# Optimization experiments

Hardware: AMD Instinct MI355X
Metric: run time of the kernel (lower is better)

Reference implementation:

```python
import jax, jax.numpy as jnp
import numpy as np

N_NODES = 50000
N_EDGES = 1600000
IN_DIM = 128
HID = 128
SHARED = 64
N_GRAPHS = 2048


def setup_inputs() -> dict:
    key = jax.random.key(0)
    ks = jax.random.split(key, 16)
    x = jax.random.normal(ks[0], (N_NODES, IN_DIM), dtype=jnp.float32)
    edge_index = jax.random.randint(ks[1], (2, N_EDGES), 0, N_NODES, dtype=jnp.int64)
    batch = jnp.sort(jax.random.randint(ks[2], (N_NODES,), 0, N_GRAPHS, dtype=jnp.int64))

    def lin(k, fan_in, fan_out):
        bound = 1.0 / np.sqrt(fan_in)
        kw, kb = jax.random.split(k)
        W = jax.random.uniform(kw, (fan_in, fan_out), minval=-bound, maxval=bound, dtype=jnp.float32)
        b = jax.random.uniform(kb, (fan_out,), minval=-bound, maxval=bound, dtype=jnp.float32)
        return W, b

    W1a, b1a = lin(ks[3], IN_DIM, HID)
    W1b, b1b = lin(ks[4], HID, HID)
    W2a, b2a = lin(ks[5], HID, HID)
    W2b, b2b = lin(ks[6], HID, HID)
    Ws, bs = lin(ks[7], HID, SHARED)
    WlS, blS = lin(ks[8], SHARED, 1)
    WlP, blP = lin(ks[9], SHARED, 1)
    WnR, bnR = lin(ks[10], SHARED, 1)
    return dict(x=x, edge_index=edge_index, batch=batch,
                W1a=W1a, b1a=b1a, W1b=W1b, b1b=b1b,
                W2a=W2a, b2a=b2a, W2b=W2b, b2b=b2b,
                Ws=Ws, bs=bs, WlS=WlS, blS=blS, WlP=WlP, blP=blP, WnR=WnR, bnR=bnR)


def gin_conv(x, src, dst, Wa, ba, Wb, bb):
    # GINConv (eps=0): h_i = MLP(x_i + sum_{j->i} x_j)
    agg = jax.ops.segment_sum(x[src], dst, num_segments=N_NODES)
    h = x + agg
    h = jax.nn.relu(h @ Wa + ba)
    return h @ Wb + bb


def reference(x, edge_index, batch, W1a, b1a, W1b, b1b, W2a, b2a, W2b, b2b,
              Ws, bs, WlS, blS, WlP, blP, WnR, bnR):
    src, dst = edge_index[0], edge_index[1]
    h = jax.nn.relu(gin_conv(x, src, dst, W1a, b1a, W1b, b1b))
    h = jax.nn.relu(gin_conv(h, src, dst, W2a, b2a, W2b, b2b))
    # global mean pool over graph ids
    sums = jax.ops.segment_sum(h, batch, num_segments=N_GRAPHS)
    counts = jax.ops.segment_sum(jnp.ones((h.shape[0],), h.dtype), batch, num_segments=N_GRAPHS)
    pooled = sums / jnp.maximum(counts, 1.0)[:, None]
    g = jax.nn.relu(pooled @ Ws + bs)
    out_logS = (g @ WlS + blS)[:, 0]
    out_logP = (g @ WlP + blP)[:, 0]
    out_NR = (g @ WnR + bnR)[:, 0]
    return (out_logS, out_logP, out_NR)
```

## Files before the change

kernel.cpp:

```cpp
#include <hip/hip_runtime.h>
#include <hip/hip_bf16.h>


#define IN_DIM 128
#define NFINE 128
#define BIN_EPB 4096
#define SRCCH 16
#define NSLOT 6400
#define SPT 13

typedef float  f32x4  __attribute__((ext_vector_type(4)));
typedef short  bf16x4 __attribute__((ext_vector_type(4)));
typedef short  bf16x8 __attribute__((ext_vector_type(8)));

__device__ __forceinline__ unsigned short bf16_rne(float v) {
    unsigned u = __float_as_uint(v);
    unsigned t = u + 0x7fffu + ((u >> 16) & 1u);
    return (unsigned short)(t >> 16);
}


__global__ __launch_bounds__(256) void f32_to_bf16_kernel(
    const float4* __restrict__ in, uint4* __restrict__ out, int n8)
{
    int i = blockIdx.x * 256 + threadIdx.x;
    if (i >= n8) return;
    float4 a = in[i * 2];
    float4 b = in[i * 2 + 1];
    float v[8] = {a.x, a.y, a.z, a.w, b.x, b.y, b.z, b.w};
    unsigned r[4];
#pragma unroll
    for (int j = 0; j < 4; ++j)
        r[j] = (unsigned)bf16_rne(v[j * 2]) | ((unsigned)bf16_rne(v[j * 2 + 1]) << 16);
    out[i] = make_uint4(r[0], r[1], r[2], r[3]);
}


__global__ __launch_bounds__(256) void conv_weights_kernel(
    const float* __restrict__ W0, const float* __restrict__ W1,
    const float* __restrict__ W2, const float* __restrict__ W3,
    unsigned short* __restrict__ Wh, unsigned short* __restrict__ Wl)
{
    int m   = blockIdx.x >> 6;
    int idx = (blockIdx.x & 63) * 256 + threadIdx.x;
    const float* W = (m == 0) ? W0 : (m == 1) ? W1 : (m == 2) ? W2 : W3;
    int k = idx >> 7, n = idx & 127;
    float v = W[idx];
    unsigned short hh = bf16_rne(v);
    float hf = __uint_as_float(((unsigned)hh) << 16);
    unsigned short ll = bf16_rne(v - hf);
    Wh[m * 16384 + n * 128 + k] = hh;
    Wl[m * 16384 + n * 128 + k] = ll;
}


__global__ __launch_bounds__(256) void bin_kernel(
    const int* __restrict__ src, const int* __restrict__ dst,
    int2* __restrict__ buckets, int* __restrict__ bcur,
    int n_edges, int n_nodes, int cap)
{
    __shared__ int cnt[NFINE];
    __shared__ int base[NFINE];
    for (int i = threadIdx.x; i < NFINE; i += 256) cnt[i] = 0;
    __syncthreads();

    const int e0 = blockIdx.x * BIN_EPB + threadIdx.x * 16;
    int ne = n_edges - e0;
    if (ne < 0) ne = 0;
    if (ne > 16) ne = 16;

    int d[16], s[16], off[16];
    if (ne == 16) {
#pragma unroll
        for (int q = 0; q < 4; ++q) {
            int4 dv = *(const int4*)(dst + e0 + q * 4);
            int4 sv = *(const int4*)(src + e0 + q * 4);
            d[q * 4 + 0] = dv.x; d[q * 4 + 1] = dv.y;
            d[q * 4 + 2] = dv.z; d[q * 4 + 3] = dv.w;
            s[q * 4 + 0] = sv.x; s[q * 4 + 1] = sv.y;
            s[q * 4 + 2] = sv.z; s[q * 4 + 3] = sv.w;
        }
    } else {
#pragma unroll
        for (int j = 0; j < 16; ++j) {
            d[j] = (j < ne) ? dst[e0 + j] : 0;
            s[j] = (j < ne) ? src[e0 + j] : 0;
        }
    }
#pragma unroll
    for (int j = 0; j < 16; ++j)
        if (j < ne) {
            int b = (int)(((long long)d[j] * NFINE) / n_nodes);
            off[j] = atomicAdd(&cnt[b], 1);
        }
    __syncthreads();
    for (int i = threadIdx.x; i < NFINE; i += 256)
        base[i] = atomicAdd(&bcur[i], cnt[i]);
    __syncthreads();
#pragma unroll
    for (int j = 0; j < 16; ++j)
        if (j < ne) {
            int b = (int)(((long long)d[j] * NFINE) / n_nodes);
            buckets[(size_t)b * cap + base[b] + off[j]] = make_int2(d[j], s[j]);
        }
}

__global__ __launch_bounds__(512) void csr_fused_kernel(
    const int2* __restrict__ buckets, const int* __restrict__ bcnt,
    int* __restrict__ row_start, int* __restrict__ csr_src,
    int cap, int n_nodes, int n_edges)
{
    __shared__ int bc[NFINE];
    __shared__ int h[NSLOT];
    __shared__ int tsum[512];
    __shared__ int bbase_s;

    const int b = blockIdx.x;
    const int t = threadIdx.x;
    const int lo_n = (int)(((long long)b * n_nodes + NFINE - 1) / NFINE);
    const int hi_n = (int)(((long long)(b + 1) * n_nodes + NFINE - 1) / NFINE);
    const int sl = hi_n - lo_n;

    if (t < NFINE) bc[t] = bcnt[t];
    for (int i = t; i < NSLOT; i += 512) h[i] = 0;
    __syncthreads();
    if (t == 0) {
        int s = 0;
        for (int i = 0; i < b; ++i) s += bc[i];
        bbase_s = s;
    }
    const int nb = bc[b];
    const int2* bp = buckets + (size_t)b * cap;
    __syncthreads();

    for (int i = t; i < nb; i += 512) {
        int2 e = bp[i];
        int key = (e.x - lo_n) * SRCCH + (int)(((long long)e.y * SRCCH) / n_nodes);
        atomicAdd(&h[key], 1);
    }
    __syncthreads();

    int base = 0;
#pragma unroll
    for (int j = 0; j < SPT; ++j) {
        int slot = t * SPT + j;
        if (slot < NSLOT) {
            int v = h[slot];
            h[slot] = base;
            base += v;
        }
    }
    tsum[t] = base;
    __syncthreads();
    int incl = tsum[t];
    for (int off = 1; off < 512; off <<= 1) {
        int tmp = (t >= off) ? tsum[t - off] : 0;
        __syncthreads();
        tsum[t] += tmp;
        __syncthreads();
        incl = tsum[t];
    }
    int texcl = incl - base + bbase_s;
#pragma unroll
    for (int j = 0; j < SPT; ++j) {
        int slot = t * SPT + j;
        if (slot < NSLOT) h[slot] += texcl;
    }
    __syncthreads();
    for (int i = t; i < sl; i += 512) row_start[lo_n + i] = h[i * SRCCH];
    if (b == NFINE - 1 && t == 0) row_start[n_nodes] = n_edges;
    __syncthreads();

    for (int i = t; i < nb; i += 512) {
        int2 e = bp[i];
        int key = (e.x - lo_n) * SRCCH + (int)(((long long)e.y * SRCCH) / n_nodes);
        csr_src[atomicAdd(&h[key], 1)] = e.y;
    }
}


__device__ __forceinline__ void add_row8(float acc[8], uint4 r) {
    union { unsigned u; float f; } c;
    c.u = r.x << 16;         acc[0] += c.f;
    c.u = r.x & 0xffff0000u; acc[1] += c.f;
    c.u = r.y << 16;         acc[2] += c.f;
    c.u = r.y & 0xffff0000u; acc[3] += c.f;
    c.u = r.z << 16;         acc[4] += c.f;
    c.u = r.z & 0xffff0000u; acc[5] += c.f;
    c.u = r.w << 16;         acc[6] += c.f;
    c.u = r.w & 0xffff0000u; acc[7] += c.f;
}

__global__ __launch_bounds__(256) void gather_agg_bf16_kernel(
    const float* __restrict__ xf,
    const uint4* __restrict__ xb,
    const int* __restrict__ row_start, const int* __restrict__ csr_src,
    float* __restrict__ out, int n_nodes)
{
    int t = blockIdx.x * 256 + threadIdx.x;
    int node = t >> 4;
    int lane = t & 15;
    if (node >= n_nodes) return;
    int lo = row_start[node];
    int hi = row_start[node + 1];

    const f32x4* xfr = (const f32x4*)(xf + (size_t)node * IN_DIM + lane * 8);
    f32x4 a0 = __builtin_nontemporal_load(xfr);
    f32x4 a1 = __builtin_nontemporal_load(xfr + 1);
    float acc[8] = {a0.x, a0.y, a0.z, a0.w, a1.x, a1.y, a1.z, a1.w};

    int e = lo;
    for (; e + 3 < hi; e += 4) {
        int s0 = csr_src[e];
        int s1 = csr_src[e + 1];
        int s2 = csr_src[e + 2];
        int s3 = csr_src[e + 3];
        uint4 r0 = xb[(size_t)s0 * 16 + lane];
        uint4 r1 = xb[(size_t)s1 * 16 + lane];
        uint4 r2 = xb[(size_t)s2 * 16 + lane];
        uint4 r3 = xb[(size_t)s3 * 16 + lane];
        add_row8(acc, r0);
        add_row8(acc, r1);
        add_row8(acc, r2);
        add_row8(acc, r3);
    }
    for (; e < hi; ++e) {
        uint4 r = xb[(size_t)csr_src[e] * 16 + lane];
        add_row8(acc, r);
    }

    f32x4 o0 = {acc[0], acc[1], acc[2], acc[3]};
    f32x4 o1 = {acc[4], acc[5], acc[6], acc[7]};
    f32x4* op = (f32x4*)(out + (size_t)node * IN_DIM + lane * 8);
    __builtin_nontemporal_store(o0, op);
    __builtin_nontemporal_store(o1, op + 1);
}

#define HSTRIDE 132

template <bool EMIT_BF16>
__global__ __launch_bounds__(256) void fused_mlp_kernel(
    const float* __restrict__ A,
    const unsigned short* __restrict__ Wa_h, const unsigned short* __restrict__ Wa_l,
    const float* __restrict__ ba,
    const unsigned short* __restrict__ Wb_h, const unsigned short* __restrict__ Wb_l,
    const float* __restrict__ bb,
    float* __restrict__ C, unsigned short* __restrict__ Cb, int M)
{
    __shared__ __align__(16) unsigned short Hh[64][HSTRIDE];
    __shared__ __align__(16) unsigned short Hl[64][HSTRIDE];

    const int t    = threadIdx.x;
    const int wave = t >> 6;
    const int lane = t & 63;
    const int l15  = lane & 15;
    const int quad = lane >> 4;
    const int rw   = (wave & 1) * 32;
    const int cw   = (wave >> 1) * 64;
    const int row0 = blockIdx.x * 64 + rw;

    f32x4 acc[2][4];
#pragma unroll
    for (int ti = 0; ti < 2; ++ti)
#pragma unroll
        for (int ct = 0; ct < 4; ++ct) acc[ti][ct] = {0.f, 0.f, 0.f, 0.f};

    {
        int ar0 = row0 + l15;
        int ar1 = row0 + 16 + l15;
        const float* ap0 = A + (size_t)((ar0 < M) ? ar0 : (M - 1)) * IN_DIM + quad * 8;
        const float* ap1 = A + (size_t)((ar1 < M) ? ar1 : (M - 1)) * IN_DIM + quad * 8;
#pragma unroll
        for (int k0 = 0; k0 < IN_DIM; k0 += 32) {
            bf16x8 ah[2], al[2];
#pragma unroll
            for (int ti = 0; ti < 2; ++ti) {
                const float* ap = ti ? ap1 : ap0;
                f32x4 v0 = *(const f32x4*)(ap + k0);
                f32x4 v1 = *(const f32x4*)(ap + k0 + 4);
                float v[8] = {v0.x, v0.y, v0.z, v0.w, v1.x, v1.y, v1.z, v1.w};
                unsigned short h[8], l[8];
#pragma unroll
                for (int j = 0; j < 8; ++j) {
                    unsigned short hh = bf16_rne(v[j]);
                    h[j] = hh;
                    l[j] = bf16_rne(v[j] - __uint_as_float(((unsigned)hh) << 16));
                }
                ah[ti] = *(const bf16x8*)h;
                al[ti] = *(const bf16x8*)l;
            }
#pragma unroll
            for (int ct = 0; ct < 4; ++ct) {
                const size_t woff = (size_t)(cw + ct * 16 + l15) * IN_DIM + k0 + quad * 8;
                bf16x8 wh = *(const bf16x8*)(Wa_h + woff);
                bf16x8 wl = *(const bf16x8*)(Wa_l + woff);
                acc[0][ct] = __builtin_amdgcn_mfma_f32_16x16x32_bf16(ah[0], wh, acc[0][ct], 0, 0, 0);
                acc[1][ct] = __builtin_amdgcn_mfma_f32_16x16x32_bf16(ah[1], wh, acc[1][ct], 0, 0, 0);
                acc[0][ct] = __builtin_amdgcn_mfma_f32_16x16x32_bf16(al[0], wh, acc[0][ct], 0, 0, 0);
                acc[1][ct] = __builtin_amdgcn_mfma_f32_16x16x32_bf16(al[1], wh, acc[1][ct], 0, 0, 0);
                acc[0][ct] = __builtin_amdgcn_mfma_f32_16x16x32_bf16(ah[0], wl, acc[0][ct], 0, 0, 0);
                acc[1][ct] = __builtin_amdgcn_mfma_f32_16x16x32_bf16(ah[1], wl, acc[1][ct], 0, 0, 0);
            }
        }
    }

#pragma unroll
    for (int ti = 0; ti < 2; ++ti) {
#pragma unroll
        for (int ct = 0; ct < 4; ++ct) {
            int col = cw + ct * 16 + l15;
            float b = ba[col];
#pragma unroll
            for (int r = 0; r < 4; ++r) {
                int rl = rw + ti * 16 + quad * 4 + r;
                float v = fmaxf(acc[ti][ct][r] + b, 0.f);
                unsigned short hh = bf16_rne(v);
                Hh[rl][col] = hh;
                Hl[rl][col] = bf16_rne(v - __uint_as_float(((unsigned)hh) << 16));
            }
            acc[ti][ct] = {0.f, 0.f, 0.f, 0.f};
        }
    }
    __syncthreads();

#pragma unroll
    for (int k0 = 0; k0 < IN_DIM; k0 += 32) {
        const int hk = k0 + quad * 8;
        bf16x8 ah[2], al[2];
#pragma unroll
        for (int ti = 0; ti < 2; ++ti) {
            const int hr = rw + ti * 16 + l15;
            bf16x4 h0 = *(const bf16x4*)&Hh[hr][hk];
            bf16x4 h1 = *(const bf16x4*)&Hh[hr][hk + 4];
            bf16x4 l0 = *(const bf16x4*)&Hl[hr][hk];
            bf16x4 l1 = *(const bf16x4*)&Hl[hr][hk + 4];
            ah[ti] = __builtin_shufflevector(h0, h1, 0, 1, 2, 3, 4, 5, 6, 7);
            al[ti] = __builtin_shufflevector(l0, l1, 0, 1, 2, 3, 4, 5, 6, 7);
        }
#pragma unroll
        for (int ct = 0; ct < 4; ++ct) {
            const size_t woff = (size_t)(cw + ct * 16 + l15) * IN_DIM + k0 + quad * 8;
            bf16x8 wh = *(const bf16x8*)(Wb_h + woff);
            bf16x8 wl = *(const bf16x8*)(Wb_l + woff);
            acc[0][ct] = __builtin_amdgcn_mfma_f32_16x16x32_bf16(ah[0], wh, acc[0][ct], 0, 0, 0);
            acc[1][ct] = __builtin_amdgcn_mfma_f32_16x16x32_bf16(ah[1], wh, acc[1][ct], 0, 0, 0);
            acc[0][ct] = __builtin_amdgcn_mfma_f32_16x16x32_bf16(al[0], wh, acc[0][ct], 0, 0, 0);
            acc[1][ct] = __builtin_amdgcn_mfma_f32_16x16x32_bf16(al[1], wh, acc[1][ct], 0, 0, 0);
            acc[0][ct] = __builtin_amdgcn_mfma_f32_16x16x32_bf16(ah[0], wl, acc[0][ct], 0, 0, 0);
            acc[1][ct] = __builtin_amdgcn_mfma_f32_16x16x32_bf16(ah[1], wl, acc[1][ct], 0, 0, 0);
        }
    }

#pragma unroll
    for (int ti = 0; ti < 2; ++ti) {
        const int rbase = row0 + ti * 16 + quad * 4;
#pragma unroll
        for (int ct = 0; ct < 4; ++ct) {
            int col = cw + ct * 16 + l15;
            float b = bb[col];
#pragma unroll
            for (int r = 0; r < 4; ++r) {
                int row = rbase + r;
                if (row < M) {
                    float o = fmaxf(acc[ti][ct][r] + b, 0.f);
                    C[(size_t)row * IN_DIM + col] = o;
                    if (EMIT_BF16)
                        Cb[(size_t)row * IN_DIM + col] = bf16_rne(o);
                }
            }
        }
    }
}


__device__ __forceinline__ int lower_bound_i(const int* __restrict__ a, int n, int v) {
    int lo = 0, hi = n;
    while (lo < hi) {
        int mid = (lo + hi) >> 1;
        if (a[mid] < v) lo = mid + 1; else hi = mid;
    }
    return lo;
}

__global__ __launch_bounds__(128) void pool_kernel(
    const float* __restrict__ h, const int* __restrict__ batch,
    float* __restrict__ pooled, int n_nodes, int n_graphs)
{
    int g = blockIdx.x;
    int lo = lower_bound_i(batch, n_nodes, g);
    int hi = lower_bound_i(batch, n_nodes, g + 1);
    int j = threadIdx.x;
    float acc = 0.f;
    for (int i = lo; i < hi; ++i)
        acc += h[(size_t)i * IN_DIM + j];
    float cnt = (float)(hi - lo);
    pooled[(size_t)g * IN_DIM + j] = acc / fmaxf(cnt, 1.0f);
}

__global__ __launch_bounds__(64) void head_kernel(
    const float* __restrict__ pooled,
    const float* __restrict__ Ws,  const float* __restrict__ bs,
    const float* __restrict__ WlS, const float* __restrict__ blS,
    const float* __restrict__ WlP, const float* __restrict__ blP,
    const float* __restrict__ WnR, const float* __restrict__ bnR,
    float* __restrict__ out, int n_graphs)
{
    int g = blockIdx.x;
    int j = threadIdx.x;
    const float* p = pooled + (size_t)g * IN_DIM;
    float acc = bs[j];
#pragma unroll 8
    for (int k = 0; k < IN_DIM; ++k)
        acc = fmaf(p[k], Ws[k * 64 + j], acc);
    float gj = fmaxf(acc, 0.f);
    float s1 = gj * WlS[j];
    float s2 = gj * WlP[j];
    float s3 = gj * WnR[j];
#pragma unroll
    for (int off = 32; off > 0; off >>= 1) {
        s1 += __shfl_down(s1, off);
        s2 += __shfl_down(s2, off);
        s3 += __shfl_down(s3, off);
    }
    if (j == 0) {
        out[g]                = s1 + blS[0];
        out[n_graphs + g]     = s2 + blP[0];
        out[2 * n_graphs + g] = s3 + bnR[0];
    }
}


extern "C" void kernel_launch(void* const* d_in, const int* in_sizes, int n_in,
                              void* d_out, int out_size, void* d_ws, size_t ws_size,
                              hipStream_t stream)
{
    const float* x   = (const float*)d_in[0];
    const int*   ei  = (const int*)d_in[1];
    const int*   bat = (const int*)d_in[2];
    const float* W1a = (const float*)d_in[3];
    const float* b1a = (const float*)d_in[4];
    const float* W1b = (const float*)d_in[5];
    const float* b1b = (const float*)d_in[6];
    const float* W2a = (const float*)d_in[7];
    const float* b2a = (const float*)d_in[8];
    const float* W2b = (const float*)d_in[9];
    const float* b2b = (const float*)d_in[10];
    const float* Ws  = (const float*)d_in[11];
    const float* bs  = (const float*)d_in[12];
    const float* WlS = (const float*)d_in[13];
    const float* blS = (const float*)d_in[14];
    const float* WlP = (const float*)d_in[15];
    const float* blP = (const float*)d_in[16];
    const float* WnR = (const float*)d_in[17];
    const float* bnR = (const float*)d_in[18];

    const int n_nodes  = in_sizes[0] / IN_DIM;
    const int n_edges  = in_sizes[1] / 2;
    const int n_graphs = out_size / 3;
    const int* src = ei;
    const int* dst = ei + n_edges;

    const size_t node_elems   = (size_t)n_nodes * IN_DIM;
    const size_t pooled_elems = (size_t)n_graphs * IN_DIM;

    float* xbf    = (float*)d_ws;
    float* buf2   = xbf  + node_elems;
    float* bufA   = buf2 + node_elems;
    float* pooled = bufA + node_elems;
    int* row_start = (int*)(pooled + pooled_elems);
    int* bcur      = row_start + (n_nodes + 1);
    int* csr_src   = bcur + NFINE;
    unsigned short* wt_h = (unsigned short*)(csr_src + n_edges);
    unsigned short* wt_l = wt_h + 4 * 16384;

    unsigned short* xb = (unsigned short*)xbf;
    const int cap = n_edges / NFINE + 2048;
    int2* buckets = (int2*)bufA;

    const int gatherblocks = (int)(((size_t)n_nodes * 16 + 255) / 256);
    const int mlpblocks = (n_nodes + 63) / 64;
    const int binblocks = (n_edges + BIN_EPB - 1) / BIN_EPB;
    const int n8 = (int)(node_elems / 8);
    const int cvtblocks = (n8 + 255) / 256;

    conv_weights_kernel<<<256, 256, 0, stream>>>(W1a, W1b, W2a, W2b, wt_h, wt_l);
    hipMemsetAsync(bcur, 0, NFINE * sizeof(int), stream);
    bin_kernel<<<binblocks, 256, 0, stream>>>(src, dst, buckets, bcur,
                                              n_edges, n_nodes, cap);
    csr_fused_kernel<<<NFINE, 512, 0, stream>>>(buckets, bcur, row_start,
                                                csr_src, cap, n_nodes, n_edges);

    f32_to_bf16_kernel<<<cvtblocks, 256, 0, stream>>>((const float4*)x, (uint4*)xb, n8);
    gather_agg_bf16_kernel<<<gatherblocks, 256, 0, stream>>>(
        x, (const uint4*)xb, row_start, csr_src, bufA, n_nodes);
    fused_mlp_kernel<true><<<mlpblocks, 256, 0, stream>>>(
        bufA, wt_h, wt_l, b1a, wt_h + 16384, wt_l + 16384, b1b,
        buf2, xb, n_nodes);

    gather_agg_bf16_kernel<<<gatherblocks, 256, 0, stream>>>(
        buf2, (const uint4*)xb, row_start, csr_src, bufA, n_nodes);
    fused_mlp_kernel<false><<<mlpblocks, 256, 0, stream>>>(
        bufA, wt_h + 2 * 16384, wt_l + 2 * 16384, b2a,
        wt_h + 3 * 16384, wt_l + 3 * 16384, b2b,
        buf2, nullptr, n_nodes);

    pool_kernel<<<n_graphs, 128, 0, stream>>>(buf2, bat, pooled, n_nodes, n_graphs);
    head_kernel<<<n_graphs, 64, 0, stream>>>(pooled, Ws, bs, WlS, blS, WlP, blP,
                                             WnR, bnR, (float*)d_out, n_graphs);
}
```

Measured before the change: 372.9 us.

## Pack bucket edges into 32-bit words, double bucket count, hoist MLP loads

The edge binning now stores each edge as a single 32-bit word: the destination offset within its bucket goes in the high 16 bits and the source id in the low 16 bits. This halves bucket traffic, and the bucket count doubles to 256, which shrinks the per-bucket shared histogram. In the fused MLP kernel, all A-row and weight fragments are loaded up front, ahead of the MFMA chains, to expose more memory-level parallelism. The cost is higher register pressure, and the 16-bit packing relies on node ids fitting below 65536, which holds for 50000 nodes but is not general.

```diff
diff --git a/kernel.cpp b/kernel.cpp
--- a/kernel.cpp
+++ b/kernel.cpp
@@ -3,11 +3,11 @@
 
 
 #define IN_DIM 128
-#define NFINE 128
+#define NFINE 256
 #define BIN_EPB 4096
 #define SRCCH 16
-#define NSLOT 6400
-#define SPT 13
+#define NSLOT 3200
+#define SPT 7
 
 typedef float  f32x4  __attribute__((ext_vector_type(4)));
 typedef short  bf16x4 __attribute__((ext_vector_type(4)));
@@ -54,14 +54,18 @@
 }
 
 
+__device__ __forceinline__ int bucket_lo(int b, int n_nodes) {
+    return (int)(((long long)b * n_nodes + NFINE - 1) / NFINE);
+}
+
 __global__ __launch_bounds__(256) void bin_kernel(
     const int* __restrict__ src, const int* __restrict__ dst,
-    int2* __restrict__ buckets, int* __restrict__ bcur,
+    int* __restrict__ buckets, int* __restrict__ bcur,
     int n_edges, int n_nodes, int cap)
 {
     __shared__ int cnt[NFINE];
     __shared__ int base[NFINE];
-    for (int i = threadIdx.x; i < NFINE; i += 256) cnt[i] = 0;
+    cnt[threadIdx.x] = 0;
     __syncthreads();
 
     const int e0 = blockIdx.x * BIN_EPB + threadIdx.x * 16;
@@ -94,19 +98,19 @@
             off[j] = atomicAdd(&cnt[b], 1);
         }
     __syncthreads();
-    for (int i = threadIdx.x; i < NFINE; i += 256)
-        base[i] = atomicAdd(&bcur[i], cnt[i]);
+    base[threadIdx.x] = atomicAdd(&bcur[threadIdx.x], cnt[threadIdx.x]);
     __syncthreads();
 #pragma unroll
     for (int j = 0; j < 16; ++j)
         if (j < ne) {
             int b = (int)(((long long)d[j] * NFINE) / n_nodes);
-            buckets[(size_t)b * cap + base[b] + off[j]] = make_int2(d[j], s[j]);
+            int pack = ((d[j] - bucket_lo(b, n_nodes)) << 16) | s[j];
+            buckets[(size_t)b * cap + base[b] + off[j]] = pack;
         }
 }
 
 __global__ __launch_bounds__(512) void csr_fused_kernel(
-    const int2* __restrict__ buckets, const int* __restrict__ bcnt,
+    const int* __restrict__ buckets, const int* __restrict__ bcnt,
     int* __restrict__ row_start, int* __restrict__ csr_src,
     int cap, int n_nodes, int n_edges)
 {
@@ -117,8 +121,8 @@
 
     const int b = blockIdx.x;
     const int t = threadIdx.x;
-    const int lo_n = (int)(((long long)b * n_nodes + NFINE - 1) / NFINE);
-    const int hi_n = (int)(((long long)(b + 1) * n_nodes + NFINE - 1) / NFINE);
+    const int lo_n = bucket_lo(b, n_nodes);
+    const int hi_n = bucket_lo(b + 1, n_nodes);
     const int sl = hi_n - lo_n;
 
     if (t < NFINE) bc[t] = bcnt[t];
@@ -130,12 +134,12 @@
         bbase_s = s;
     }
     const int nb = bc[b];
-    const int2* bp = buckets + (size_t)b * cap;
+    const int* bp = buckets + (size_t)b * cap;
     __syncthreads();
 
     for (int i = t; i < nb; i += 512) {
-        int2 e = bp[i];
-        int key = (e.x - lo_n) * SRCCH + (int)(((long long)e.y * SRCCH) / n_nodes);
+        int v = bp[i];
+        int key = (v >> 16) * SRCCH + (int)(((long long)(v & 0xFFFF) * SRCCH) / n_nodes);
         atomicAdd(&h[key], 1);
     }
     __syncthreads();
@@ -152,15 +156,13 @@
     }
     tsum[t] = base;
     __syncthreads();
-    int incl = tsum[t];
     for (int off = 1; off < 512; off <<= 1) {
         int tmp = (t >= off) ? tsum[t - off] : 0;
         __syncthreads();
         tsum[t] += tmp;
         __syncthreads();
-        incl = tsum[t];
-    }
-    int texcl = incl - base + bbase_s;
+    }
+    int texcl = tsum[t] - base + bbase_s;
 #pragma unroll
     for (int j = 0; j < SPT; ++j) {
         int slot = t * SPT + j;
@@ -172,9 +174,9 @@
     __syncthreads();
 
     for (int i = t; i < nb; i += 512) {
-        int2 e = bp[i];
-        int key = (e.x - lo_n) * SRCCH + (int)(((long long)e.y * SRCCH) / n_nodes);
-        csr_src[atomicAdd(&h[key], 1)] = e.y;
+        int v = bp[i];
+        int key = (v >> 16) * SRCCH + (int)(((long long)(v & 0xFFFF) * SRCCH) / n_nodes);
+        csr_src[atomicAdd(&h[key], 1)] = v & 0xFFFF;
     }
 }
 
@@ -259,48 +261,59 @@
     const int cw   = (wave >> 1) * 64;
     const int row0 = blockIdx.x * 64 + rw;
 
+    bf16x8 ah[2][4], al[2][4];
+
+#pragma unroll
+    for (int ti = 0; ti < 2; ++ti) {
+        int ar = row0 + ti * 16 + l15;
+        const float* ap = A + (size_t)((ar < M) ? ar : (M - 1)) * IN_DIM + quad * 8;
+        f32x4 av[8];
+#pragma unroll
+        for (int k0c = 0; k0c < 4; ++k0c) {
+            av[k0c * 2]     = *(const f32x4*)(ap + k0c * 32);
+            av[k0c * 2 + 1] = *(const f32x4*)(ap + k0c * 32 + 4);
+        }
+#pragma unroll
+        for (int k0c = 0; k0c < 4; ++k0c) {
+            float v[8] = {av[k0c * 2].x, av[k0c * 2].y, av[k0c * 2].z, av[k0c * 2].w,
+                          av[k0c * 2 + 1].x, av[k0c * 2 + 1].y,
+                          av[k0c * 2 + 1].z, av[k0c * 2 + 1].w};
+            unsigned short hh[8], ll[8];
+#pragma unroll
+            for (int j = 0; j < 8; ++j) {
+                unsigned short h = bf16_rne(v[j]);
+                hh[j] = h;
+                ll[j] = bf16_rne(v[j] - __uint_as_float(((unsigned)h) << 16));
+            }
+            ah[ti][k0c] = *(const bf16x8*)hh;
+            al[ti][k0c] = *(const bf16x8*)ll;
+        }
+    }
+
     f32x4 acc[2][4];
 #pragma unroll
     for (int ti = 0; ti < 2; ++ti)
 #pragma unroll
         for (int ct = 0; ct < 4; ++ct) acc[ti][ct] = {0.f, 0.f, 0.f, 0.f};
 
-    {
-        int ar0 = row0 + l15;
-        int ar1 = row0 + 16 + l15;
-        const float* ap0 = A + (size_t)((ar0 < M) ? ar0 : (M - 1)) * IN_DIM + quad * 8;
-        const float* ap1 = A + (size_t)((ar1 < M) ? ar1 : (M - 1)) * IN_DIM + quad * 8;
-#pragma unroll
-        for (int k0 = 0; k0 < IN_DIM; k0 += 32) {
-            bf16x8 ah[2], al[2];
-#pragma unroll
-            for (int ti = 0; ti < 2; ++ti) {
-                const float* ap = ti ? ap1 : ap0;
-                f32x4 v0 = *(const f32x4*)(ap + k0);
-                f32x4 v1 = *(const f32x4*)(ap + k0 + 4);
-                float v[8] = {v0.x, v0.y, v0.z, v0.w, v1.x, v1.y, v1.z, v1.w};
-                unsigned short h[8], l[8];
-#pragma unroll
-                for (int j = 0; j < 8; ++j) {
-                    unsigned short hh = bf16_rne(v[j]);
-                    h[j] = hh;
-                    l[j] = bf16_rne(v[j] - __uint_as_float(((unsigned)hh) << 16));
-                }
-                ah[ti] = *(const bf16x8*)h;
-                al[ti] = *(const bf16x8*)l;
-            }
-#pragma unroll
-            for (int ct = 0; ct < 4; ++ct) {
-                const size_t woff = (size_t)(cw + ct * 16 + l15) * IN_DIM + k0 + quad * 8;
-                bf16x8 wh = *(const bf16x8*)(Wa_h + woff);
-                bf16x8 wl = *(const bf16x8*)(Wa_l + woff);
-                acc[0][ct] = __builtin_amdgcn_mfma_f32_16x16x32_bf16(ah[0], wh, acc[0][ct], 0, 0, 0);
-                acc[1][ct] = __builtin_amdgcn_mfma_f32_16x16x32_bf16(ah[1], wh, acc[1][ct], 0, 0, 0);
-                acc[0][ct] = __builtin_amdgcn_mfma_f32_16x16x32_bf16(al[0], wh, acc[0][ct], 0, 0, 0);
-                acc[1][ct] = __builtin_amdgcn_mfma_f32_16x16x32_bf16(al[1], wh, acc[1][ct], 0, 0, 0);
-                acc[0][ct] = __builtin_amdgcn_mfma_f32_16x16x32_bf16(ah[0], wl, acc[0][ct], 0, 0, 0);
-                acc[1][ct] = __builtin_amdgcn_mfma_f32_16x16x32_bf16(ah[1], wl, acc[1][ct], 0, 0, 0);
-            }
+#pragma unroll
+    for (int ct = 0; ct < 4; ++ct) {
+        const unsigned short* wph = Wa_h + (size_t)(cw + ct * 16 + l15) * IN_DIM + quad * 8;
+        const unsigned short* wpl = Wa_l + (size_t)(cw + ct * 16 + l15) * IN_DIM + quad * 8;
+        bf16x8 wh[4], wl[4];
+#pragma unroll
+        for (int k0c = 0; k0c < 4; ++k0c) {
+            wh[k0c] = *(const bf16x8*)(wph + k0c * 32);
+            wl[k0c] = *(const bf16x8*)(wpl + k0c * 32);
+        }
+#pragma unroll
+        for (int k0c = 0; k0c < 4; ++k0c) {
+            acc[0][ct] = __builtin_amdgcn_mfma_f32_16x16x32_bf16(ah[0][k0c], wh[k0c], acc[0][ct], 0, 0, 0);
+            acc[1][ct] = __builtin_amdgcn_mfma_f32_16x16x32_bf16(ah[1][k0c], wh[k0c], acc[1][ct], 0, 0, 0);
+            acc[0][ct] = __builtin_amdgcn_mfma_f32_16x16x32_bf16(al[0][k0c], wh[k0c], acc[0][ct], 0, 0, 0);
+            acc[1][ct] = __builtin_amdgcn_mfma_f32_16x16x32_bf16(al[1][k0c], wh[k0c], acc[1][ct], 0, 0, 0);
+            acc[0][ct] = __builtin_amdgcn_mfma_f32_16x16x32_bf16(ah[0][k0c], wl[k0c], acc[0][ct], 0, 0, 0);
+            acc[1][ct] = __builtin_amdgcn_mfma_f32_16x16x32_bf16(ah[1][k0c], wl[k0c], acc[1][ct], 0, 0, 0);
         }
     }
 
@@ -324,30 +337,38 @@
     __syncthreads();
 
 #pragma unroll
-    for (int k0 = 0; k0 < IN_DIM; k0 += 32) {
-        const int hk = k0 + quad * 8;
-        bf16x8 ah[2], al[2];
-#pragma unroll
-        for (int ti = 0; ti < 2; ++ti) {
-            const int hr = rw + ti * 16 + l15;
+    for (int ti = 0; ti < 2; ++ti) {
+        const int hr = rw + ti * 16 + l15;
+#pragma unroll
+        for (int k0c = 0; k0c < 4; ++k0c) {
+            const int hk = k0c * 32 + quad * 8;
             bf16x4 h0 = *(const bf16x4*)&Hh[hr][hk];
             bf16x4 h1 = *(const bf16x4*)&Hh[hr][hk + 4];
             bf16x4 l0 = *(const bf16x4*)&Hl[hr][hk];
             bf16x4 l1 = *(const bf16x4*)&Hl[hr][hk + 4];
-            ah[ti] = __builtin_shufflevector(h0, h1, 0, 1, 2, 3, 4, 5, 6, 7);
-            al[ti] = __builtin_shufflevector(l0, l1, 0, 1, 2, 3, 4, 5, 6, 7);
-        }
-#pragma unroll
-        for (int ct = 0; ct < 4; ++ct) {
-            const size_t woff = (size_t)(cw + ct * 16 + l15) * IN_DIM + k0 + quad * 8;
-            bf16x8 wh = *(const bf16x8*)(Wb_h + woff);
-            bf16x8 wl = *(const bf16x8*)(Wb_l + woff);
-            acc[0][ct] = __builtin_amdgcn_mfma_f32_16x16x32_bf16(ah[0], wh, acc[0][ct], 0, 0, 0);
-            acc[1][ct] = __builtin_amdgcn_mfma_f32_16x16x32_bf16(ah[1], wh, acc[1][ct], 0, 0, 0);
-            acc[0][ct] = __builtin_amdgcn_mfma_f32_16x16x32_bf16(al[0], wh, acc[0][ct], 0, 0, 0);
-            acc[1][ct] = __builtin_amdgcn_mfma_f32_16x16x32_bf16(al[1], wh, acc[1][ct], 0, 0, 0);
-            acc[0][ct] = __builtin_amdgcn_mfma_f32_16x16x32_bf16(ah[0], wl, acc[0][ct], 0, 0, 0);
-            acc[1][ct] = __builtin_amdgcn_mfma_f32_16x16x32_bf16(ah[1], wl, acc[1][ct], 0, 0, 0);
+            ah[ti][k0c] = __builtin_shufflevector(h0, h1, 0, 1, 2, 3, 4, 5, 6, 7);
+            al[ti][k0c] = __builtin_shufflevector(l0, l1, 0, 1, 2, 3, 4, 5, 6, 7);
+        }
+    }
+
+#pragma unroll
+    for (int ct = 0; ct < 4; ++ct) {
+        const unsigned short* wph = Wb_h + (size_t)(cw + ct * 16 + l15) * IN_DIM + quad * 8;
+        const unsigned short* wpl = Wb_l + (size_t)(cw + ct * 16 + l15) * IN_DIM + quad * 8;
+        bf16x8 wh[4], wl[4];
+#pragma unroll
+        for (int k0c = 0; k0c < 4; ++k0c) {
+            wh[k0c] = *(const bf16x8*)(wph + k0c * 32);
+            wl[k0c] = *(const bf16x8*)(wpl + k0c * 32);
+        }
+#pragma unroll
+        for (int k0c = 0; k0c < 4; ++k0c) {
+            acc[0][ct] = __builtin_amdgcn_mfma_f32_16x16x32_bf16(ah[0][k0c], wh[k0c], acc[0][ct], 0, 0, 0);
+            acc[1][ct] = __builtin_amdgcn_mfma_f32_16x16x32_bf16(ah[1][k0c], wh[k0c], acc[1][ct], 0, 0, 0);
+            acc[0][ct] = __builtin_amdgcn_mfma_f32_16x16x32_bf16(al[0][k0c], wh[k0c], acc[0][ct], 0, 0, 0);
+            acc[1][ct] = __builtin_amdgcn_mfma_f32_16x16x32_bf16(al[1][k0c], wh[k0c], acc[1][ct], 0, 0, 0);
+            acc[0][ct] = __builtin_amdgcn_mfma_f32_16x16x32_bf16(ah[0][k0c], wl[k0c], acc[0][ct], 0, 0, 0);
+            acc[1][ct] = __builtin_amdgcn_mfma_f32_16x16x32_bf16(ah[1][k0c], wl[k0c], acc[1][ct], 0, 0, 0);
         }
     }
 
@@ -474,8 +495,8 @@
     unsigned short* wt_l = wt_h + 4 * 16384;
 
     unsigned short* xb = (unsigned short*)xbf;
-    const int cap = n_edges / NFINE + 2048;
-    int2* buckets = (int2*)bufA;
+    const int cap = n_edges / NFINE + 1024;
+    int* buckets = (int*)bufA;
 
     const int gatherblocks = (int)(((size_t)n_nodes * 16 + 255) / 256);
     const int mlpblocks = (n_nodes + 63) / 64;
```

New measurement: 375.8 us. Within noise of the previous version (+0.8%).
